# Kernel tuning notes

Hardware: AMD Instinct MI355X
Metric: run time of the kernel (lower is better)

Reference implementation:

```python
import jax, jax.numpy as jnp
import numpy as np

BN_EPS = 1e-5

def _conv1x1(x, w, b=None):
    # x: [B,C,H,W], w: [O,C] -> [B,O,H,W]
    y = jnp.einsum('bchw,oc->bohw', x, w)
    if b is not None:
        y = y + b[None, :, None, None]
    return y

def _bn_silu(y, gamma, beta):
    # BN inference with running_mean=0, running_var=1, then SiLU
    scale = gamma / jnp.sqrt(1.0 + BN_EPS)
    y = y * scale[None, :, None, None] + beta[None, :, None, None]
    return jax.nn.silu(y)

def setup_inputs() -> dict:
    key = jax.random.key(0)
    ks = jax.random.split(key, 20)
    B, D, S = 32, 512, 32
    C = D // 2
    d = {}
    d['x'] = jax.random.normal(ks[0], (B, D, S, S), jnp.float32)
    d['cv1_w'] = jax.random.normal(ks[1], (C, D), jnp.float32) * (1.0 / np.sqrt(D))
    d['cv1_gamma'] = jax.random.uniform(ks[2], (C,), jnp.float32, 0.5, 1.5)
    d['cv1_beta'] = jax.random.normal(ks[3], (C,), jnp.float32) * 0.1
    d['q_w'] = jax.random.normal(ks[4], (C, C), jnp.float32) * (1.0 / np.sqrt(C))
    d['q_b'] = jax.random.normal(ks[5], (C,), jnp.float32) * 0.02
    d['k_w'] = jax.random.normal(ks[6], (C, C), jnp.float32) * (1.0 / np.sqrt(C))
    d['k_b'] = jax.random.normal(ks[7], (C,), jnp.float32) * 0.02
    d['v_w'] = jax.random.normal(ks[8], (C, C), jnp.float32) * (1.0 / np.sqrt(C))
    d['v_b'] = jax.random.normal(ks[9], (C,), jnp.float32) * 0.02
    d['e_w'] = jax.random.normal(ks[10], (C, C), jnp.float32) * (1.0 / np.sqrt(C))
    d['e_b'] = jax.random.normal(ks[11], (C,), jnp.float32) * 0.02
    d['rel_h'] = jax.random.normal(ks[12], (1, C, S, 1), jnp.float32)
    d['rel_w'] = jax.random.normal(ks[13], (1, C, 1, S), jnp.float32)
    d['cv2_w'] = jax.random.normal(ks[14], (D, C), jnp.float32) * (1.0 / np.sqrt(C))
    d['cv2_gamma'] = jax.random.uniform(ks[15], (D,), jnp.float32, 0.5, 1.5)
    d['cv2_beta'] = jax.random.normal(ks[16], (D,), jnp.float32) * 0.1
    return d

def reference(x, cv1_w, cv1_gamma, cv1_beta, q_w, q_b, k_w, k_b, v_w, v_b,
              e_w, e_b, rel_h, rel_w, cv2_w, cv2_gamma, cv2_beta):
    # cv1: 1x1 conv (no bias) + BN + SiLU
    x1 = _bn_silu(_conv1x1(x, cv1_w), cv1_gamma, cv1_beta)  # [B,C,H,W]
    B, C, H, W = x1.shape
    N = H * W
    q = _conv1x1(x1, q_w, q_b).reshape(B, C, N)
    k = _conv1x1(x1, k_w, k_b).reshape(B, C, N)
    v = _conv1x1(x1, v_w, v_b).reshape(B, C, N)
    e = _conv1x1(x1, e_w, e_b).reshape(B, C, N)
    # content-content: q^T k -> [B,N,N]
    cc = jnp.einsum('bci,bcj->bij', q, k)
    # content-position: (rel_h + rel_w) flattened to [C,N], times extra proj
    pos = (rel_h + rel_w).reshape(C, N)  # broadcast add -> [1,C,H,W] -> [C,N]
    cp = jnp.einsum('ci,bcj->bij', pos, e)  # [B,N,N]
    attn = jax.nn.softmax(cc + cp, axis=-1)
    # out[b,c,i] = sum_j v[b,c,j] * attn[b,i,j]
    out = jnp.einsum('bcj,bij->bci', v, attn).reshape(B, C, H, W)
    y = _bn_silu(_conv1x1(out, cv2_w), cv2_gamma, cv2_beta)
    return x + y
```

## Files before the change

### kernel.cpp

```cpp
#include <hip/hip_runtime.h>
#include <hip/hip_bf16.h>

typedef unsigned short u16;
typedef __attribute__((ext_vector_type(8))) _Float16 half8;
typedef __attribute__((ext_vector_type(4))) float f32x4;

__device__ __forceinline__ u16 f2h(float f) {
  _Float16 h = (_Float16)f;
  union { _Float16 h; u16 u; } a; a.h = h;
  return a.u;
}

__device__ __forceinline__ float h2f(u16 u) {
  union { _Float16 h; u16 u; } a; a.u = u;
  return (float)a.h;
}

__device__ __forceinline__ float silu_f(float y) {
  return y / (1.0f + __expf(-y));
}

__device__ __forceinline__ void glds16(const u16* g, u16* l) {
  __builtin_amdgcn_global_load_lds(
      (__attribute__((address_space(1))) unsigned*)(g),
      (__attribute__((address_space(3))) unsigned*)(l), 16, 0, 0);
}

enum { EPI_BNSILU_N = 0, EPI_QKEV, EPI_RAW_F16, EPI_BNSILU_RES_M };

template<int EPI, bool DUAL, int TILES, int GX>
__global__ __launch_bounds__(256, 4)
void gemm_nt(const u16* __restrict__ A, long long a_bs, int lda,
             const u16* __restrict__ A2,
             const u16* __restrict__ B, long long b_bs, int ldb,
             void* __restrict__ C0, long long c_bs, int ldc,
             void* __restrict__ C1, void* __restrict__ C2,
             int K,
             const float* __restrict__ p0, const float* __restrict__ p1,
             const float* __restrict__ res, long long res_bs)
{
  __shared__ u16 smem[8192];
  u16* lA = smem;
  u16* lB = smem + 4096;

  const int id = blockIdx.x;
  const int bz = (id & 7) + 8 * (id / (8 * TILES));
  const int tt = (id >> 3) % TILES;
  const int bm = tt % GX;
  const int bn = tt / GX;
  const u16* Ab = A + (long long)bz * a_bs;
  const u16* Bb = B + (long long)bz * b_bs;
  const int m0 = bm * 128;
  const int n0 = bn * 128;
  const int t = threadIdx.x;
  const int lane = t & 63;
  const int w = t >> 6;
  const int wm = (w & 1) * 64;
  const int wn = (w >> 1) * 64;
  const int q = lane >> 4;
  const int lr = lane & 15;

  f32x4 acc[4][4];
#pragma unroll
  for (int i = 0; i < 4; ++i)
#pragma unroll
    for (int j = 0; j < 4; ++j)
      acc[i][j] = (f32x4){0.f, 0.f, 0.f, 0.f};

  const int lrow = lane >> 2;
  const int kch = (lane & 3) ^ ((lane >> 2) & 3) ^ ((lane >> 4) & 3);
  const int lk = kch * 8;
  const u16* aR0 = Ab + (long long)(m0 + 32 * w + lrow) * lda + lk;
  const u16* aR1 = aR0 + 16LL * lda;
  const u16* bR0 = Bb + (long long)(n0 + 32 * w + lrow) * ldb + lk;
  const u16* bR1 = bR0 + 16LL * ldb;
  const u16* a2R0 = nullptr; const u16* a2R1 = nullptr;
  if constexpr (DUAL) {
    a2R0 = A2 + (long long)(m0 + 32 * w + lrow) * 256 + lk;
    a2R1 = a2R0 + 16LL * 256;
  }
  u16* la0 = lA + w * 1024; u16* la1 = la0 + 512;
  u16* lb0 = lB + w * 1024; u16* lb1 = lb0 + 512;
  const int fpos = (q ^ (lr & 3) ^ ((lr >> 2) & 3)) * 8;

  for (int k0 = 0; k0 < K; k0 += 32) {
    __syncthreads();
    if (!DUAL || k0 < 256) {
      glds16(aR0 + k0, la0);
      glds16(aR1 + k0, la1);
    } else {
      glds16(a2R0 + (k0 - 256), la0);
      glds16(a2R1 + (k0 - 256), la1);
    }
    glds16(bR0 + k0, lb0);
    glds16(bR1 + k0, lb1);
    __syncthreads();
    half8 af[4], bfr[4];
#pragma unroll
    for (int i = 0; i < 4; ++i)
      af[i] = *(const half8*)&lA[(wm + i * 16 + lr) * 32 + fpos];
#pragma unroll
    for (int j = 0; j < 4; ++j)
      bfr[j] = *(const half8*)&lB[(wn + j * 16 + lr) * 32 + fpos];
#pragma unroll
    for (int i = 0; i < 4; ++i)
#pragma unroll
      for (int j = 0; j < 4; ++j)
        acc[i][j] = __builtin_amdgcn_mfma_f32_16x16x32_f16(af[i], bfr[j], acc[i][j], 0, 0, 0);
  }

  if constexpr (EPI == EPI_BNSILU_N) {
    u16* Cg = (u16*)C0 + (long long)bz * c_bs;
#pragma unroll
    for (int i = 0; i < 4; ++i)
#pragma unroll
      for (int j = 0; j < 4; ++j)
#pragma unroll
        for (int r = 0; r < 4; ++r) {
          const int m = m0 + wm + i * 16 + q * 4 + r;
          const int n = n0 + wn + j * 16 + lr;
          float v = acc[i][j][r];
          v = silu_f(v * (p0[n] * 0.99999500003749969f) + p1[n]);
          Cg[(long long)m * ldc + n] = f2h(v);
        }
  } else if constexpr (EPI == EPI_RAW_F16) {
    u16* Cg = (u16*)C0 + (long long)bz * c_bs;
#pragma unroll
    for (int i = 0; i < 4; ++i)
#pragma unroll
      for (int j = 0; j < 4; ++j)
#pragma unroll
        for (int r = 0; r < 4; ++r) {
          const int m = m0 + wm + i * 16 + q * 4 + r;
          const int n = n0 + wn + j * 16 + lr;
          Cg[(long long)m * ldc + n] = f2h(acc[i][j][r]);
        }
  } else if constexpr (EPI == EPI_BNSILU_RES_M) {
    float* Cg = (float*)C0 + (long long)bz * c_bs;
    const float* rg = res + (long long)bz * res_bs;
#pragma unroll
    for (int i = 0; i < 4; ++i)
#pragma unroll
      for (int j = 0; j < 4; ++j)
#pragma unroll
        for (int r = 0; r < 4; ++r) {
          const int m = m0 + wm + i * 16 + q * 4 + r;
          const int n = n0 + wn + j * 16 + lr;
          float v = acc[i][j][r];
          v = silu_f(v * (p0[m] * 0.99999500003749969f) + p1[m]);
          const long long idx = (long long)m * ldc + n;
          Cg[idx] = v + rg[idx];
        }
  } else {
    const int seg = n0 >> 8;
    const int nb = n0 & 255;
    if (seg < 3) {
      u16* dst; long long bs; int ld2;
      if (seg == 0) { dst = (u16*)C0; bs = 262144; ld2 = 256; }
      else { dst = (u16*)C1 + (seg == 2 ? 256 : 0); bs = 524288; ld2 = 512; }
      dst += (long long)bz * bs;
#pragma unroll
      for (int i = 0; i < 4; ++i)
#pragma unroll
        for (int j = 0; j < 4; ++j)
#pragma unroll
          for (int r = 0; r < 4; ++r) {
            const int m = m0 + wm + i * 16 + q * 4 + r;
            const int col = wn + j * 16 + lr;
            float v = acc[i][j][r] + p0[n0 + col];
            dst[(long long)m * ld2 + nb + col] = f2h(v);
          }
    } else {
      u16* dst = (u16*)C2 + (long long)bz * 262144;
#pragma unroll
      for (int s = 0; s < 4; ++s) {
        const int rbase = s * 32;
        __syncthreads();
        if (wm == (rbase & 64)) {
          const int ibase = (rbase & 32) >> 4;
#pragma unroll
          for (int ii = 0; ii < 2; ++ii) {
            const int i = ibase + ii;
#pragma unroll
            for (int j = 0; j < 4; ++j)
#pragma unroll
              for (int r = 0; r < 4; ++r) {
                const int row32 = i * 16 + q * 4 + r - (rbase & 32);
                const int col = wn + j * 16 + lr;
                float v = acc[i][j][r] + p0[768 + nb + col];
                smem[row32 * 132 + col] = f2h(v);
              }
          }
        }
        __syncthreads();
#pragma unroll
        for (int p = 0; p < 2; ++p) {
          const int lin = p * 256 + t;
          const int c = lin >> 2;
          const int mc = lin & 3;
          u16 tmp[8];
#pragma unroll
          for (int r8 = 0; r8 < 8; ++r8)
            tmp[r8] = smem[(mc * 8 + r8) * 132 + c];
          *(half8*)&dst[(long long)(nb + c) * 1024 + m0 + rbase + mc * 8] =
              *(const half8*)tmp;
        }
      }
    }
  }
}

__global__ __launch_bounds__(256)
void transpose_x(const float* __restrict__ x, u16* __restrict__ xT) {
  __shared__ float tile[64][33];
  const int b = blockIdx.z;
  const int n0 = blockIdx.x * 32;
  const int d0 = blockIdx.y * 64;
  const int tx = threadIdx.x;
  const int ty = threadIdx.y;
  const float* src = x + (long long)b * 524288;
#pragma unroll
  for (int i = 0; i < 8; ++i)
    tile[ty + 8 * i][tx] = src[(long long)(d0 + ty + 8 * i) * 1024 + n0 + tx];
  __syncthreads();
  u16* dst = xT + (long long)b * 524288;
#pragma unroll
  for (int i = 0; i < 4; ++i) {
    const int n = ty + 8 * i;
    unsigned lo = (unsigned)f2h(tile[2 * tx][n]);
    unsigned hi = (unsigned)f2h(tile[2 * tx + 1][n]);
    *(unsigned*)&dst[(long long)(n0 + n) * 512 + d0 + 2 * tx] = lo | (hi << 16);
  }
}

__global__ __launch_bounds__(256)
void convert_w(const float* __restrict__ w1, const float* __restrict__ wq,
               const float* __restrict__ wk, const float* __restrict__ wv,
               const float* __restrict__ we, const float* __restrict__ w2,
               const float* __restrict__ bq, const float* __restrict__ bk,
               const float* __restrict__ be, const float* __restrict__ bv,
               u16* __restrict__ dstw, float* __restrict__ bbuf) {
  int id = blockIdx.x * 256 + threadIdx.x;
  if (id < 524288) {
    float v;
    if (id < 131072) v = w1[id];
    else if (id < 393216) {
      int s = id - 131072, o = s >> 8, c = s & 255;
      if (o < 256) v = wq[o * 256 + c];
      else if (o < 512) v = wk[(o - 256) * 256 + c];
      else if (o < 768) v = we[(o - 512) * 256 + c];
      else v = wv[(o - 768) * 256 + c];
    } else v = w2[id - 393216];
    dstw[id] = f2h(v);
  } else {
    int i = id - 524288;
    float v;
    if (i < 256) v = bq[i];
    else if (i < 512) v = bk[i - 256];
    else if (i < 768) v = be[i - 512];
    else v = bv[i - 768];
    bbuf[i] = v;
  }
}

__global__ __launch_bounds__(256)
void pos_compute(const float* __restrict__ rh, const float* __restrict__ rw,
                 u16* __restrict__ posT) {
  const int n = blockIdx.x;
  const int c = threadIdx.x;
  posT[n * 256 + c] = f2h(rh[c * 32 + (n >> 5)] + rw[c * 32 + (n & 31)]);
}

__global__ __launch_bounds__(256)
void softmax_rows(u16* __restrict__ logits) {
  __shared__ float red[8];
  u16* p = logits + (long long)blockIdx.x * 1024;
  const int t = threadIdx.x;
  ushort4 raw = ((const ushort4*)p)[t];
  float v0 = h2f(raw.x), v1 = h2f(raw.y), v2 = h2f(raw.z), v3 = h2f(raw.w);
  float mx = fmaxf(fmaxf(v0, v1), fmaxf(v2, v3));
#pragma unroll
  for (int off = 32; off > 0; off >>= 1) mx = fmaxf(mx, __shfl_down(mx, off));
  const int lane = t & 63, w = t >> 6;
  if (lane == 0) red[w] = mx;
  __syncthreads();
  mx = fmaxf(fmaxf(red[0], red[1]), fmaxf(red[2], red[3]));
  float e0 = __expf(v0 - mx), e1 = __expf(v1 - mx),
        e2 = __expf(v2 - mx), e3 = __expf(v3 - mx);
  float s = e0 + e1 + e2 + e3;
#pragma unroll
  for (int off = 32; off > 0; off >>= 1) s += __shfl_down(s, off);
  if (lane == 0) red[4 + w] = s;
  __syncthreads();
  const float inv = 1.0f / (red[4] + red[5] + red[6] + red[7]);
  ushort4 o;
  o.x = f2h(e0 * inv); o.y = f2h(e1 * inv); o.z = f2h(e2 * inv); o.w = f2h(e3 * inv);
  ((ushort4*)p)[t] = o;
}

extern "C" void kernel_launch(void* const* d_in, const int* in_sizes, int n_in,
                              void* d_out, int out_size, void* d_ws, size_t ws_size,
                              hipStream_t stream) {
  const float* x  = (const float*)d_in[0];
  const float* w1 = (const float*)d_in[1];
  const float* g1 = (const float*)d_in[2];
  const float* b1 = (const float*)d_in[3];
  const float* wq = (const float*)d_in[4];
  const float* bq = (const float*)d_in[5];
  const float* wk = (const float*)d_in[6];
  const float* bk = (const float*)d_in[7];
  const float* wv = (const float*)d_in[8];
  const float* bv = (const float*)d_in[9];
  const float* we = (const float*)d_in[10];
  const float* be = (const float*)d_in[11];
  const float* rh = (const float*)d_in[12];
  const float* rw = (const float*)d_in[13];
  const float* w2 = (const float*)d_in[14];
  const float* g2 = (const float*)d_in[15];
  const float* b2 = (const float*)d_in[16];
  float* out = (float*)d_out;
  char* ws = (char*)d_ws;

  u16* xT     = (u16*)(ws + 0);
  u16* x1t    = (u16*)(ws + 33554432);
  u16* qbuf   = (u16*)(ws + 50331648);
  u16* kcat   = (u16*)(ws + 67108864);
  u16* vbuf   = (u16*)(ws + 100663296);
  u16* outt   = (u16*)(ws + 117440512);
  u16* posT   = (u16*)(ws + 134217728);
  u16* wbuf   = (u16*)(ws + 134742016);
  float* bbuf = (float*)(ws + 135790592);
  u16* logits = (u16*)(ws + 142606336);

  u16* w1b    = wbuf;
  u16* wqkve  = wbuf + 131072;
  u16* w2b    = wbuf + 393216;

  transpose_x<<<dim3(32, 8, 32), dim3(32, 8), 0, stream>>>(x, xT);
  convert_w<<<dim3(2052), 256, 0, stream>>>(w1, wq, wk, wv, we, w2,
                                            bq, bk, be, bv, wbuf, bbuf);
  pos_compute<<<dim3(1024), 256, 0, stream>>>(rh, rw, posT);

  gemm_nt<EPI_BNSILU_N, false, 16, 8><<<dim3(512), 256, 0, stream>>>(
      xT, 524288LL, 512, nullptr, w1b, 0LL, 512,
      x1t, 262144LL, 256, nullptr, nullptr, 512, g1, b1, nullptr, 0LL);

  gemm_nt<EPI_QKEV, false, 64, 8><<<dim3(2048), 256, 0, stream>>>(
      x1t, 262144LL, 256, nullptr, wqkve, 0LL, 256,
      qbuf, 262144LL, 256, kcat, vbuf, 256, bbuf, nullptr, nullptr, 0LL);

  gemm_nt<EPI_RAW_F16, true, 64, 8><<<dim3(2048), 256, 0, stream>>>(
      qbuf, 262144LL, 256, posT, kcat, 524288LL, 512,
      logits, 1048576LL, 1024, nullptr, nullptr, 512, nullptr, nullptr, nullptr, 0LL);

  softmax_rows<<<dim3(32768), 256, 0, stream>>>(logits);

  gemm_nt<EPI_RAW_F16, false, 16, 8><<<dim3(512), 256, 0, stream>>>(
      logits, 1048576LL, 1024, nullptr, vbuf, 262144LL, 1024,
      outt, 262144LL, 256, nullptr, nullptr, 1024, nullptr, nullptr, nullptr, 0LL);

  gemm_nt<EPI_BNSILU_RES_M, false, 32, 4><<<dim3(1024), 256, 0, stream>>>(
      w2b, 0LL, 256, nullptr, outt, 262144LL, 256,
      out, 524288LL, 1024, nullptr, nullptr, 256, g2, b2, x, 524288LL);
}
```

Baseline: 337.7 us.

## Double-buffer GEMM LDS staging with 64-wide K steps and MFMA priority

```diff
diff --git a/kernel.cpp b/kernel.cpp
--- a/kernel.cpp
+++ b/kernel.cpp
@@ -29,7 +29,7 @@
 enum { EPI_BNSILU_N = 0, EPI_QKEV, EPI_RAW_F16, EPI_BNSILU_RES_M };
 
 template<int EPI, bool DUAL, int TILES, int GX>
-__global__ __launch_bounds__(256, 4)
+__global__ __launch_bounds__(256, 2)
 void gemm_nt(const u16* __restrict__ A, long long a_bs, int lda,
              const u16* __restrict__ A2,
              const u16* __restrict__ B, long long b_bs, int ldb,
@@ -39,9 +39,7 @@
              const float* __restrict__ p0, const float* __restrict__ p1,
              const float* __restrict__ res, long long res_bs)
 {
-  __shared__ u16 smem[8192];
-  u16* lA = smem;
-  u16* lB = smem + 4096;
+  __shared__ u16 smem[32768];
 
   const int id = blockIdx.x;
   const int bz = (id & 7) + 8 * (id / (8 * TILES));
@@ -79,35 +77,67 @@
     a2R0 = A2 + (long long)(m0 + 32 * w + lrow) * 256 + lk;
     a2R1 = a2R0 + 16LL * 256;
   }
-  u16* la0 = lA + w * 1024; u16* la1 = la0 + 512;
-  u16* lb0 = lB + w * 1024; u16* lb1 = lb0 + 512;
+  u16* const S0 = smem;
+  u16* const S1 = smem + 16384;
   const int fpos = (q ^ (lr & 3) ^ ((lr >> 2) & 3)) * 8;
 
-  for (int k0 = 0; k0 < K; k0 += 32) {
-    __syncthreads();
-    if (!DUAL || k0 < 256) {
-      glds16(aR0 + k0, la0);
-      glds16(aR1 + k0, la1);
-    } else {
-      glds16(a2R0 + (k0 - 256), la0);
-      glds16(a2R1 + (k0 - 256), la1);
-    }
-    glds16(bR0 + k0, lb0);
-    glds16(bR1 + k0, lb1);
-    __syncthreads();
-    half8 af[4], bfr[4];
-#pragma unroll
-    for (int i = 0; i < 4; ++i)
-      af[i] = *(const half8*)&lA[(wm + i * 16 + lr) * 32 + fpos];
-#pragma unroll
-    for (int j = 0; j < 4; ++j)
-      bfr[j] = *(const half8*)&lB[(wn + j * 16 + lr) * 32 + fpos];
-#pragma unroll
-    for (int i = 0; i < 4; ++i)
-#pragma unroll
-      for (int j = 0; j < 4; ++j)
-        acc[i][j] = __builtin_amdgcn_mfma_f32_16x16x32_f16(af[i], bfr[j], acc[i][j], 0, 0, 0);
-  }
+#define STAGE64(kk, Sb)                                                       \
+  do {                                                                        \
+    u16* _a = (Sb) + w * 1024;                                                \
+    u16* _b = (Sb) + 8192 + w * 1024;                                         \
+    if (!DUAL || (kk) < 256) {                                                \
+      glds16(aR0 + (kk), _a);            glds16(aR1 + (kk), _a + 512);        \
+      glds16(aR0 + (kk) + 32, _a + 4096); glds16(aR1 + (kk) + 32, _a + 4608); \
+    } else {                                                                  \
+      glds16(a2R0 + ((kk) - 256), _a);   glds16(a2R1 + ((kk) - 256), _a + 512);\
+      glds16(a2R0 + ((kk) - 224), _a + 4096);                                 \
+      glds16(a2R1 + ((kk) - 224), _a + 4608);                                 \
+    }                                                                         \
+    glds16(bR0 + (kk), _b);            glds16(bR1 + (kk), _b + 512);          \
+    glds16(bR0 + (kk) + 32, _b + 4096); glds16(bR1 + (kk) + 32, _b + 4608);   \
+  } while (0)
+
+#define COMPUTE64(Sb)                                                         \
+  do {                                                                        \
+    _Pragma("unroll")                                                         \
+    for (int h = 0; h < 2; ++h) {                                             \
+      half8 af[4], bfr[4];                                                    \
+      _Pragma("unroll")                                                       \
+      for (int i = 0; i < 4; ++i)                                             \
+        af[i] = *(const half8*)&(Sb)[h * 4096 + (wm + i * 16 + lr) * 32 + fpos];\
+      _Pragma("unroll")                                                       \
+      for (int j = 0; j < 4; ++j)                                             \
+        bfr[j] = *(const half8*)&(Sb)[8192 + h * 4096 + (wn + j * 16 + lr) * 32 + fpos];\
+      __builtin_amdgcn_s_setprio(1);                                          \
+      _Pragma("unroll")                                                       \
+      for (int i = 0; i < 4; ++i)                                             \
+        _Pragma("unroll")                                                     \
+        for (int j = 0; j < 4; ++j)                                           \
+          acc[i][j] = __builtin_amdgcn_mfma_f32_16x16x32_f16(af[i], bfr[j],   \
+                                                             acc[i][j], 0,0,0);\
+      __builtin_amdgcn_s_setprio(0);                                          \
+    }                                                                         \
+  } while (0)
+
+#define PHASE_END()                                                           \
+  do {                                                                        \
+    asm volatile("s_waitcnt vmcnt(0) lgkmcnt(0)" ::: "memory");               \
+    __builtin_amdgcn_s_barrier();                                             \
+  } while (0)
+
+  STAGE64(0, S0);
+  PHASE_END();
+  for (int k0 = 0; k0 < K; k0 += 128) {
+    if (k0 + 64 < K) STAGE64(k0 + 64, S1);
+    COMPUTE64(S0);
+    PHASE_END();
+    if (k0 + 128 < K) STAGE64(k0 + 128, S0);
+    COMPUTE64(S1);
+    PHASE_END();
+  }
+#undef STAGE64
+#undef COMPUTE64
+#undef PHASE_END
 
   if constexpr (EPI == EPI_BNSILU_N) {
     u16* Cg = (u16*)C0 + (long long)bz * c_bs;
```

Result: no change. 332.1 us (-1.7%).
